# Kernel optimization log

Measured on AMD Instinct MI355X. Metric: run time of the kernel, lower is better.

## Reference

```python
import jax, jax.numpy as jnp
import numpy as np

SR = 44100
SEQ_DUR = 6.0
FBINS = 113
FMIN = 91.6
NSGT_SCALE = 100.0
MIN_WIN = 4


def _mel_frequencies(fmin, fmax, bnds):
    # MelScale from the nsgt package
    hz2mel = lambda f: 1127.01048 * np.log(f / 700.0 + 1.0)
    mel2hz = lambda m: (np.exp(m / 1127.01048) - 1.0) * 700.0
    mmin, mmax = hz2mel(fmin), hz2mel(fmax)
    mbnd = (mmax - mmin) / (bnds - 1)
    return mel2hz(np.arange(bnds) * mbnd + mmin)


def _hannwin(l):
    # fft-centered hann window (peak at index 0), as in nsgt.util.hannwin
    r = np.arange(l, dtype=np.float64) * (2.0 * np.pi / l)
    return 0.5 * (np.cos(r) + 1.0)


def _build_nsgt_params(Ls):
    """Replicates nsgfwin(sliced=False) + calcwinrange + matrixform nsgtf layout.
    Returns G[n_bins, maxLg] (window values, zero where padded) and
    idx[n_bins, maxLg] (gather indices into the length-Ls spectrum)."""
    f = _mel_frequencies(FMIN, SR / 2.0, FBINS)
    nf = SR / 2.0
    lim = int(np.argmax(f > 0))
    if lim != 0:
        f = f[lim:]
    lim = int(np.argmax(f >= nf))
    if lim != 0:
        f = f[:lim]
    lbas = len(f)
    frqs = np.concatenate(((0.0,), f, (nf,)))
    fbas = np.concatenate((frqs, SR - frqs[-2:0:-1]))
    fbas *= float(Ls) / SR
    # bandwidths M[k] (samples)
    M = np.zeros(fbas.shape, dtype=np.int64)
    M[0] = np.round(2 * fbas[1])
    for k in range(1, 2 * lbas + 1):
        M[k] = np.round(fbas[k + 1] - fbas[k - 1])
    M[-1] = np.round(Ls - fbas[-2])
    M = np.clip(M, MIN_WIN, None)
    g = [_hannwin(m) for m in M]
    fbas[lbas] = (fbas[lbas - 1] + fbas[lbas + 1]) / 2
    fbas[lbas + 2] = Ls - fbas[lbas]
    rfbas = np.round(fbas).astype(np.int64)  # window center positions (= timepos)
    # real=True, reducedform=0 -> keep bins 0 .. len(g)//2 (DC..Nyquist)
    n_bins = len(g) // 2 + 1
    maxLg = int(M.max())  # matrixform: every bin padded (in the middle) to max bandwidth
    idx = np.zeros((n_bins, maxLg), dtype=np.int32)
    G = np.zeros((n_bins, maxLg), dtype=np.float32)
    for j in range(n_bins):
        gj = g[j]
        Lg = len(gj)
        tp = int(rfbas[j])
        h = (Lg + 1) // 2  # positive-frequency half
        nh = Lg // 2       # negative-frequency half
        idx[j, :h] = (tp + np.arange(h)) % Ls
        G[j, :h] = gj[:h]
        if nh > 0:
            idx[j, maxLg - nh:] = (tp - nh + np.arange(nh)) % Ls
            G[j, maxLg - nh:] = gj[h:]
    return G, idx


def setup_inputs() -> dict:
    key = jax.random.key(0)
    S, C = 16, 2
    Ls = int(SEQ_DUR * SR)
    x = jax.random.normal(key, (S, C, Ls), dtype=jnp.float32)
    G, idx = _build_nsgt_params(Ls)
    return {"x": x, "G": jnp.asarray(G), "idx": jnp.asarray(idx)}


def reference(x, G, idx):
    # x: (S, C, Ls); G, idx: (n_bins, maxLg)
    S, C, T = x.shape
    ft = jnp.fft.fft(x.reshape(S * C, T))      # (N, Ls) complex64
    c = ft[:, idx] * G                         # (N, n_bins, maxLg): windowed spectrum slices
    coefs = jnp.fft.ifft(c, axis=-1)           # per-bin time frames (matrixform NSGT coeffs)
    coefs = coefs.reshape(S, C, c.shape[1], c.shape[2])
    # torch.view_as_real + * NSGT_SCALE
    return jnp.stack([coefs.real, coefs.imag], axis=-1) * NSGT_SCALE
```

## Files before the change

kernel.cpp:

```cpp
#include <hip/hip_runtime.h>

#define TPB 256
#define TPF 1024
constexpr int LS = 264600;
constexpr int N1 = 525;
constexpr int N2 = 504;
constexpr int ROWS = 32;
constexpr int M_FFT = 16384;
constexpr float TWO_PI_F = 6.28318530717958647692f;
constexpr float PI_F     = 3.14159265358979323846f;

__device__ __forceinline__ int rev7(int x) { return (int)(__brev((unsigned)x) >> 25); }
__device__ __forceinline__ float2 cmul(float2 a, float2 b) {
    return make_float2(a.x * b.x - a.y * b.y, a.x * b.y + a.y * b.x);
}
__device__ __forceinline__ int sidx(int hi, int lo) {
    return (hi << 7) + (lo ^ (hi & 15));
}

__global__ void k0_scan(const float* __restrict__ G, int NL, int* __restrict__ hnh) {
    const int j = blockIdx.x;
    __shared__ int s_first, s_last;
    if (threadIdx.x == 0) { s_first = NL; s_last = -1; }
    __syncthreads();
    const float* Gj = G + (size_t)j * NL;
    for (int m = threadIdx.x; m < NL; m += blockDim.x) {
        if (Gj[m] == 0.0f) {
            atomicMin(&s_first, m);
            atomicMax(&s_last, m);
        }
    }
    __syncthreads();
    if (threadIdx.x == 0) {
        int h  = s_first;
        int nh = (s_last >= 0) ? (NL - 1 - s_last) : 0;
        hnh[2 * j]     = h;
        hnh[2 * j + 1] = nh;
    }
}

__global__ __launch_bounds__(TPB) void k1_dft525(const float* __restrict__ x,
                                                 float2* __restrict__ A) {
    const int n2 = blockIdx.x;
    const int r  = blockIdx.y;
    __shared__ float  xs[N1];
    __shared__ float2 ys[N1];
    __shared__ float2 w25[25];
    __shared__ float2 w21[21];
    const float* xr = x + (size_t)r * LS + n2;
    for (int t = threadIdx.x; t < N1; t += TPB) {
        xs[t] = xr[(size_t)t * N2];
    }
    if (threadIdx.x < 25) {
        float a = -TWO_PI_F * (float)threadIdx.x / 25.0f;
        float s, c; sincosf(a, &s, &c);
        w25[threadIdx.x] = make_float2(c, s);
    } else if (threadIdx.x >= 32 && threadIdx.x < 53) {
        int k = threadIdx.x - 32;
        float a = -TWO_PI_F * (float)k / 21.0f;
        float s, c; sincosf(a, &s, &c);
        w21[k] = make_float2(c, s);
    }
    __syncthreads();
    for (int i = threadIdx.x; i < N1; i += TPB) {
        int alpha = i % 25, b = i / 25;
        float re = 0.f, im = 0.f;
        int iw = 0, it = b;
        #pragma unroll
        for (int a = 0; a < 25; ++a) {
            float  v = xs[it];
            float2 w = w25[iw];
            re = fmaf(v, w.x, re);
            im = fmaf(v, w.y, im);
            it += 21;
            iw += alpha; if (iw >= 25) iw -= 25;
        }
        float ang = -TWO_PI_F * (float)(b * alpha) / (float)N1;
        float s, c; sincosf(ang, &s, &c);
        ys[i] = make_float2(re * c - im * s, re * s + im * c);
    }
    __syncthreads();
    for (int k = threadIdx.x; k < N1; k += TPB) {
        int alpha = k % 25, beta = k / 25;
        float re = 0.f, im = 0.f;
        int iw = 0, iy = alpha;
        #pragma unroll
        for (int b = 0; b < 21; ++b) {
            float2 v = ys[iy];
            float2 w = w21[iw];
            re = fmaf(v.x, w.x, re); re = fmaf(-v.y, w.y, re);
            im = fmaf(v.x, w.y, im); im = fmaf( v.y, w.x, im);
            iy += 25;
            iw += beta; if (iw >= 21) iw -= 21;
        }
        float ang = -TWO_PI_F * (float)(k * n2) / (float)LS;
        float s, c; sincosf(ang, &s, &c);
        A[((size_t)r * N1 + k) * N2 + n2] = make_float2(re * c - im * s, re * s + im * c);
    }
}

__global__ __launch_bounds__(TPB) void k2_dft504(float2* __restrict__ A) {
    const int k1 = blockIdx.x;
    const int r  = blockIdx.y;
    __shared__ float2 as[N2];
    __shared__ float2 ys[N2];
    __shared__ float2 w21[21];
    __shared__ float2 w24[24];
    float2* row = A + ((size_t)r * N1 + k1) * N2;
    for (int t = threadIdx.x; t < N2; t += TPB) as[t] = row[t];
    if (threadIdx.x < 21) {
        float a = -TWO_PI_F * (float)threadIdx.x / 21.0f;
        float s, c; sincosf(a, &s, &c);
        w21[threadIdx.x] = make_float2(c, s);
    } else if (threadIdx.x >= 32 && threadIdx.x < 56) {
        int k = threadIdx.x - 32;
        float a = -TWO_PI_F * (float)k / 24.0f;
        float s, c; sincosf(a, &s, &c);
        w24[k] = make_float2(c, s);
    }
    __syncthreads();
    for (int i = threadIdx.x; i < N2; i += TPB) {
        int alpha = i % 21, b = i / 21;
        float re = 0.f, im = 0.f;
        int iw = 0, it = b;
        #pragma unroll
        for (int a = 0; a < 21; ++a) {
            float2 v = as[it];
            float2 w = w21[iw];
            re = fmaf(v.x, w.x, re); re = fmaf(-v.y, w.y, re);
            im = fmaf(v.x, w.y, im); im = fmaf( v.y, w.x, im);
            it += 24;
            iw += alpha; if (iw >= 21) iw -= 21;
        }
        float ang = -TWO_PI_F * (float)(b * alpha) / (float)N2;
        float s, c; sincosf(ang, &s, &c);
        ys[i] = make_float2(re * c - im * s, re * s + im * c);
    }
    __syncthreads();
    for (int k = threadIdx.x; k < N2; k += TPB) {
        int alpha = k % 21, beta = k / 21;
        float re = 0.f, im = 0.f;
        int iw = 0, iy = alpha;
        #pragma unroll
        for (int b = 0; b < 24; ++b) {
            float2 v = ys[iy];
            float2 w = w24[iw];
            re = fmaf(v.x, w.x, re); re = fmaf(-v.y, w.y, re);
            im = fmaf(v.x, w.y, im); im = fmaf( v.y, w.x, im);
            iy += 21;
            iw += beta; if (iw >= 24) iw -= 24;
        }
        row[k] = make_float2(re, im);
    }
}

__global__ void k_setup(float2* __restrict__ kc, float2* __restrict__ bchirp,
                        float2* __restrict__ twg, int NL) {
    int t = blockIdx.x * blockDim.x + threadIdx.x;
    long long twoNL = 2LL * NL;
    if (t < M_FFT) {
        long long d = 0; bool act = false;
        if (t < NL)              { d = t;        act = true; }
        else if (t > M_FFT - NL) { d = t - M_FFT; act = true; }
        float2 v = make_float2(0.f, 0.f);
        if (act) {
            long long ph = (d * d) % twoNL;
            float th = -PI_F * (float)ph / (float)NL;
            float s, c; sincosf(th, &s, &c);
            v = make_float2(c, s);
        }
        kc[t] = v;
    } else {
        int n = t - M_FFT;
        if (n < NL) {
            long long ph = ((long long)n * n) % twoNL;
            float th = PI_F * (float)ph / (float)NL;
            float s, c; sincosf(th, &s, &c);
            bchirp[n] = make_float2(c, s);
        } else if (n < NL + 64) {
            int q = n - NL;
            float th = -TWO_PI_F * (float)q / 128.0f;
            float s, c; sincosf(th, &s, &c);
            twg[q] = make_float2(c, s);
        }
    }
}

__device__ void fft128_dif(float2 (*ld)[129], const float2* tw, int f, int q) {
    for (int ls = 6; ls >= 0; --ls) {
        int span = 1 << ls;
        for (int b = q; b < 64; b += 16) {
            int j = b & (span - 1);
            int g = b >> ls;
            int u = (g << (ls + 1)) + j;
            int v = u + span;
            float2 A = ld[f][u], B = ld[f][v];
            float2 s = make_float2(A.x + B.x, A.y + B.y);
            float2 d = make_float2(A.x - B.x, A.y - B.y);
            ld[f][u] = s;
            ld[f][v] = cmul(d, tw[j << (6 - ls)]);
        }
        __syncthreads();
    }
}

#define FFT_PROLOG                                                        \
    __shared__ float2 ld[16][129];                                        \
    __shared__ float2 tw[64];                                             \
    if (threadIdx.x < 64) {                                               \
        float th = -TWO_PI_F * (float)threadIdx.x / 128.0f;               \
        float s, c; sincosf(th, &s, &c);                                  \
        tw[threadIdx.x] = make_float2(c, s);                              \
    }

__global__ __launch_bounds__(TPB) void kfft_cols_fwd(float2* __restrict__ P) {
    const int cg = blockIdx.x;
    const size_t vb = (size_t)blockIdx.y * M_FFT;
    FFT_PROLOG
    const int c0 = cg * 16;
    for (int i = threadIdx.x; i < 2048; i += TPB) {
        int cl = i & 15, r = i >> 4;
        ld[cl][r] = P[vb + (c0 + cl) + 128 * r];
    }
    __syncthreads();
    fft128_dif(ld, tw, threadIdx.x >> 4, threadIdx.x & 15);
    for (int i = threadIdx.x; i < 2048; i += TPB) {
        int cl = i & 15, pos = i >> 4;
        int c = c0 + cl;
        int k1 = rev7(pos);
        float th = -TWO_PI_F * (float)(c * k1) / (float)M_FFT;
        float s, co; sincosf(th, &s, &co);
        P[vb + c + 128 * pos] = cmul(ld[cl][pos], make_float2(co, s));
    }
}

__global__ __launch_bounds__(TPB) void kfft_rows_fwd(float2* __restrict__ P) {
    const int rg = blockIdx.x;
    const size_t vb = (size_t)blockIdx.y * M_FFT;
    FFT_PROLOG
    const int R0 = rg * 16;
    for (int i = threadIdx.x; i < 2048; i += TPB) {
        int fl = i >> 7, c = i & 127;
        ld[fl][c] = P[vb + (size_t)(R0 + fl) * 128 + c];
    }
    __syncthreads();
    fft128_dif(ld, tw, threadIdx.x >> 4, threadIdx.x & 15);
    for (int i = threadIdx.x; i < 2048; i += TPB) {
        int fl = i >> 7, pos = i & 127;
        P[vb + (size_t)(R0 + fl) * 128 + pos] = ld[fl][pos];
    }
}

__global__ __launch_bounds__(TPF) void k_fused(const float* __restrict__ Gm,
        const int* __restrict__ idxp, const float2* __restrict__ A,
        const int* __restrict__ hnh, const float2* __restrict__ bchirp,
        const float2* __restrict__ KF, const float2* __restrict__ twg,
        float2* __restrict__ out, int NB, int NL) {
    extern __shared__ float2 mp[];
    const int tid = threadIdx.x;
    const int vg = blockIdx.x;
    const int r = vg / NB, j = vg % NB;
    const int h = hnh[2 * j], nh = hnh[2 * j + 1];
    const int tail0 = NL - nh;
    const float* Gj = Gm + (size_t)j * NL;
    const int*   ij = idxp + (size_t)j * NL;
    const float2* Ar = A + (size_t)r * LS;

    for (int i = tid; i < M_FFT; i += TPF) {
        float2 val = make_float2(0.f, 0.f);
        if (i < h || (i >= tail0 && i < NL)) {
            int k = ij[i];
            float2 f = Ar[(size_t)(k % N1) * N2 + (k / N1)];
            float  g = Gj[i];
            val = cmul(make_float2(f.x * g, f.y * g), bchirp[i]);
        }
        mp[sidx(i >> 7, i & 127)] = val;
    }
    __syncthreads();

    for (int ls = 6; ls >= 0; --ls) {
        const int span = 1 << ls;
        for (int w = tid; w < 8192; w += TPF) {
            const int lo = w & 127, b = w >> 7;
            const int jj = b & (span - 1), g = b >> ls;
            const int u = (g << (ls + 1)) + jj, v = u + span;
            float2 Aa = mp[sidx(u, lo)], Bb = mp[sidx(v, lo)];
            float2 s = make_float2(Aa.x + Bb.x, Aa.y + Bb.y);
            float2 d = make_float2(Aa.x - Bb.x, Aa.y - Bb.y);
            mp[sidx(u, lo)] = s;
            mp[sidx(v, lo)] = cmul(d, twg[jj << (6 - ls)]);
        }
        __syncthreads();
    }
    for (int i = tid; i < M_FFT; i += TPF) {
        const int c = i & 127, pos = i >> 7;
        const int k1 = rev7(pos);
        float th = -TWO_PI_F * (float)(c * k1) / (float)M_FFT;
        float s, co; sincosf(th, &s, &co);
        const int p = sidx(pos, c);
        mp[p] = cmul(mp[p], make_float2(co, s));
    }
    __syncthreads();
    for (int ls = 6; ls >= 0; --ls) {
        const int span = 1 << ls;
        for (int w = tid; w < 8192; w += TPF) {
            const int hi = w & 127, b = w >> 7;
            const int jj = b & (span - 1), g = b >> ls;
            const int u = (g << (ls + 1)) + jj, v = u + span;
            float2 Aa = mp[sidx(hi, u)], Bb = mp[sidx(hi, v)];
            float2 s = make_float2(Aa.x + Bb.x, Aa.y + Bb.y);
            float2 d = make_float2(Aa.x - Bb.x, Aa.y - Bb.y);
            mp[sidx(hi, u)] = s;
            mp[sidx(hi, v)] = cmul(d, twg[jj << (6 - ls)]);
        }
        __syncthreads();
    }
    for (int i = tid; i < M_FFT; i += TPF) {
        const int p = sidx(i >> 7, i & 127);
        mp[p] = cmul(mp[p], KF[i]);
    }
    __syncthreads();
    for (int ls = 0; ls <= 6; ++ls) {
        const int span = 1 << ls;
        for (int w = tid; w < 8192; w += TPF) {
            const int hi = w & 127, b = w >> 7;
            const int jj = b & (span - 1), g = b >> ls;
            const int u = (g << (ls + 1)) + jj, v = u + span;
            float2 wv = twg[jj << (6 - ls)]; wv.y = -wv.y;
            float2 Aa = mp[sidx(hi, u)];
            float2 t  = cmul(mp[sidx(hi, v)], wv);
            mp[sidx(hi, u)] = make_float2(Aa.x + t.x, Aa.y + t.y);
            mp[sidx(hi, v)] = make_float2(Aa.x - t.x, Aa.y - t.y);
        }
        __syncthreads();
    }
    for (int i = tid; i < M_FFT; i += TPF) {
        const int pos = i & 127, R = i >> 7;
        const int k1 = rev7(R);
        float th = TWO_PI_F * (float)(k1 * pos) / (float)M_FFT;
        float s, co; sincosf(th, &s, &co);
        const int p = sidx(R, pos);
        mp[p] = cmul(mp[p], make_float2(co, s));
    }
    __syncthreads();
    for (int ls = 0; ls <= 6; ++ls) {
        const int span = 1 << ls;
        for (int w = tid; w < 8192; w += TPF) {
            const int lo = w & 127, b = w >> 7;
            const int jj = b & (span - 1), g = b >> ls;
            const int u = (g << (ls + 1)) + jj, v = u + span;
            float2 wv = twg[jj << (6 - ls)]; wv.y = -wv.y;
            float2 Aa = mp[sidx(u, lo)];
            float2 t  = cmul(mp[sidx(v, lo)], wv);
            mp[sidx(u, lo)] = make_float2(Aa.x + t.x, Aa.y + t.y);
            mp[sidx(v, lo)] = make_float2(Aa.x - t.x, Aa.y - t.y);
        }
        __syncthreads();
    }
    const float sc = 100.0f / ((float)NL * (float)M_FFT);
    float2* outv = out + (size_t)vg * NL;
    for (int n = tid; n < NL; n += TPF) {
        float2 y = cmul(mp[sidx(n >> 7, n & 127)], bchirp[n]);
        outv[n] = make_float2(y.x * sc, y.y * sc);
    }
}

__global__ __launch_bounds__(TPB) void k3_idft(const float* __restrict__ G,
                                               const int*  __restrict__ idxp,
                                               const float2* __restrict__ FT,
                                               const int*  __restrict__ hnh,
                                               float2* __restrict__ out,
                                               int NB, int NL) {
    extern __shared__ float2 cls[];
    const int j = blockIdx.x;
    const int r = blockIdx.y;
    const int h  = hnh[2 * j];
    const int nh = hnh[2 * j + 1];
    const int Lg = h + nh;
    const float* Gj = G    + (size_t)j * NL;
    const int*   ij = idxp + (size_t)j * NL;

    for (int t = threadIdx.x; t < Lg; t += TPB) {
        int m = (t < h) ? t : (NL - nh + (t - h));
        int k = ij[m];
        float2 f = FT[((size_t)r * N1 + (k % N1)) * N2 + (k / N1)];
        float  g = Gj[m];
        cls[t] = make_float2(f.x * g, f.y * g);
    }
    __syncthreads();

    const float scale = 100.0f / (float)NL;
    const float w0 = TWO_PI_F / (float)NL;
    float2* outr = out + ((size_t)r * NB + j) * NL;

    for (int n_base = 0; n_base < NL; n_base += 4 * TPB) {
        int   n[4];
        float are[4], aim[4], twr[4], twi[4], str[4], sti[4];
        #pragma unroll
        for (int u = 0; u < 4; ++u) {
            n[u] = n_base + u * TPB + (int)threadIdx.x;
            are[u] = 0.f; aim[u] = 0.f;
            float s, c; sincosf(w0 * (float)(n[u] % NL), &s, &c);
            str[u] = c; sti[u] = s;
            twr[u] = 1.f; twi[u] = 0.f;
        }
        for (int t = 0; t < h; ++t) {
            if ((t & 255) == 0) {
                #pragma unroll
                for (int u = 0; u < 4; ++u) {
                    int mm = (int)(((long long)t * (long long)n[u]) % NL);
                    float s, c; sincosf(w0 * (float)mm, &s, &c);
                    twr[u] = c; twi[u] = s;
                }
            }
            float2 cv = cls[t];
            #pragma unroll
            for (int u = 0; u < 4; ++u) {
                are[u] = fmaf(cv.x, twr[u], are[u]);
                are[u] = fmaf(-cv.y, twi[u], are[u]);
                aim[u] = fmaf(cv.x, twi[u], aim[u]);
                aim[u] = fmaf(cv.y, twr[u], aim[u]);
                float nr = twr[u] * str[u] - twi[u] * sti[u];
                float ni = twr[u] * sti[u] + twi[u] * str[u];
                twr[u] = nr; twi[u] = ni;
            }
        }
        const int m0 = NL - nh;
        for (int t = 0; t < nh; ++t) {
            if ((t & 255) == 0) {
                #pragma unroll
                for (int u = 0; u < 4; ++u) {
                    int mm = (int)(((long long)(m0 + t) * (long long)n[u]) % NL);
                    float s, c; sincosf(w0 * (float)mm, &s, &c);
                    twr[u] = c; twi[u] = s;
                }
            }
            float2 cv = cls[h + t];
            #pragma unroll
            for (int u = 0; u < 4; ++u) {
                are[u] = fmaf(cv.x, twr[u], are[u]);
                are[u] = fmaf(-cv.y, twi[u], are[u]);
                aim[u] = fmaf(cv.x, twi[u], aim[u]);
                aim[u] = fmaf(cv.y, twr[u], aim[u]);
                float nr = twr[u] * str[u] - twi[u] * sti[u];
                float ni = twr[u] * sti[u] + twi[u] * str[u];
                twr[u] = nr; twi[u] = ni;
            }
        }
        #pragma unroll
        for (int u = 0; u < 4; ++u) {
            if (n[u] < NL) outr[n[u]] = make_float2(are[u] * scale, aim[u] * scale);
        }
    }
}

static inline size_t align256(size_t x) { return (x + 255) & ~(size_t)255; }

extern "C" void kernel_launch(void* const* d_in, const int* in_sizes, int n_in,
                              void* d_out, int out_size, void* d_ws, size_t ws_size,
                              hipStream_t stream) {
    const float* x   = (const float*)d_in[0];
    const float* Gm  = (const float*)d_in[1];
    const int*   idx = (const int*)d_in[2];
    float2*      out = (float2*)d_out;

    const int p  = in_sizes[1];
    const int NB = (p % 114 == 0) ? 114 : 115;
    const int NL = p / NB;
    const int B  = NB * ROWS;

    size_t hnh_off    = 0;
    size_t bchirp_off = align256(hnh_off + 2048);
    size_t twg_off    = align256(bchirp_off + (size_t)NL * 8);
    size_t kc_off     = align256(twg_off + 64 * 8);
    size_t A_off      = align256(kc_off + (size_t)M_FFT * 8);
    size_t need       = A_off + (size_t)ROWS * LS * 8;

    int*    hnh    = (int*)((char*)d_ws + hnh_off);
    float2* bchirp = (float2*)((char*)d_ws + bchirp_off);
    float2* twg    = (float2*)((char*)d_ws + twg_off);
    float2* kc     = (float2*)((char*)d_ws + kc_off);
    float2* A      = (float2*)((char*)d_ws + A_off);

    k0_scan<<<dim3(NB), TPB, 0, stream>>>(Gm, NL, hnh);
    k1_dft525<<<dim3(N2, ROWS), TPB, 0, stream>>>(x, A);
    k2_dft504<<<dim3(N1, ROWS), TPB, 0, stream>>>(A);

    const bool fused_ok = (2 * NL - 1 <= M_FFT) && (need <= ws_size);
    if (fused_ok) {
        (void)hipFuncSetAttribute((const void*)k_fused,
                                  hipFuncAttributeMaxDynamicSharedMemorySize,
                                  M_FFT * (int)sizeof(float2));
        int setup_blocks = (M_FFT + NL + 64 + TPB - 1) / TPB;
        k_setup<<<dim3(setup_blocks), TPB, 0, stream>>>(kc, bchirp, twg, NL);
        kfft_cols_fwd<<<dim3(8, 1), TPB, 0, stream>>>(kc);
        kfft_rows_fwd<<<dim3(8, 1), TPB, 0, stream>>>(kc);
        k_fused<<<dim3(B), TPF, (size_t)M_FFT * sizeof(float2), stream>>>(
            Gm, idx, A, hnh, bchirp, kc, twg, out, NB, NL);
    } else {
        k3_idft<<<dim3(NB, ROWS), TPB, (size_t)NL * sizeof(float2), stream>>>(
            Gm, idx, A, hnh, out, NB, NL);
    }
}
```

Before: 1.504 ms.

## Rewrite Bluestein 16K FFT as register-resident radix-16/8 passes

Replaces the per-stage shared-memory radix-2 butterflies, which need a barrier after each of 28 stages, in the fused Bluestein kernel. Each 128-point sub-FFT is now split into an in-register radix-16 step and two radix-8 steps, with twiddles held in shared memory between them. The chirp kernel FFT moves into a single kernel that uses the same path and stores it transposed, so the pointwise multiply reads it coalesced in the new data order. The change cuts shared-memory traffic and barriers, but raises register pressure under launch_bounds(1024,4) and needs the twiddle table enlarged to 128 entries.

```diff
diff --git a/kernel.cpp b/kernel.cpp
--- a/kernel.cpp
+++ b/kernel.cpp
@@ -10,12 +10,61 @@
 constexpr float TWO_PI_F = 6.28318530717958647692f;
 constexpr float PI_F     = 3.14159265358979323846f;
 
-__device__ __forceinline__ int rev7(int x) { return (int)(__brev((unsigned)x) >> 25); }
 __device__ __forceinline__ float2 cmul(float2 a, float2 b) {
     return make_float2(a.x * b.x - a.y * b.y, a.x * b.y + a.y * b.x);
 }
 __device__ __forceinline__ int sidx(int hi, int lo) {
     return (hi << 7) + (lo ^ (hi & 15));
+}
+
+template<bool INV>
+__device__ __forceinline__ void fft16r(float2 v[16]) {
+    const float C16[8] = {1.f, 0.92387953251128674f, 0.70710678118654752f, 0.38268343236508977f,
+                          0.f, -0.38268343236508977f, -0.70710678118654752f, -0.92387953251128674f};
+    const float S16[8] = {0.f, 0.38268343236508977f, 0.70710678118654752f, 0.92387953251128674f,
+                          1.f, 0.92387953251128674f, 0.70710678118654752f, 0.38268343236508977f};
+    const float sg = INV ? 1.f : -1.f;
+    #pragma unroll
+    for (int ls = 3; ls >= 0; --ls) {
+        const int span = 1 << ls;
+        #pragma unroll
+        for (int g = 0; g < 16; g += 2 * span) {
+            #pragma unroll
+            for (int j = 0; j < span; ++j) {
+                const int u = g + j, w = u + span;
+                float2 a = v[u], b = v[w];
+                float2 d = make_float2(a.x - b.x, a.y - b.y);
+                v[u] = make_float2(a.x + b.x, a.y + b.y);
+                const int ti = j << (3 - ls);
+                v[w] = make_float2(d.x * C16[ti] - d.y * sg * S16[ti],
+                                   d.x * sg * S16[ti] + d.y * C16[ti]);
+            }
+        }
+    }
+}
+
+template<bool INV>
+__device__ __forceinline__ void fft8r(float2 v[8]) {
+    const float C8[4] = {1.f, 0.70710678118654752f, 0.f, -0.70710678118654752f};
+    const float S8[4] = {0.f, 0.70710678118654752f, 1.f, 0.70710678118654752f};
+    const float sg = INV ? 1.f : -1.f;
+    #pragma unroll
+    for (int ls = 2; ls >= 0; --ls) {
+        const int span = 1 << ls;
+        #pragma unroll
+        for (int g = 0; g < 8; g += 2 * span) {
+            #pragma unroll
+            for (int j = 0; j < span; ++j) {
+                const int u = g + j, w = u + span;
+                float2 a = v[u], b = v[w];
+                float2 d = make_float2(a.x - b.x, a.y - b.y);
+                v[u] = make_float2(a.x + b.x, a.y + b.y);
+                const int ti = j << (2 - ls);
+                v[w] = make_float2(d.x * C8[ti] - d.y * sg * S8[ti],
+                                   d.x * sg * S8[ti] + d.y * C8[ti]);
+            }
+        }
+    }
 }
 
 __global__ void k0_scan(const float* __restrict__ G, int NL, int* __restrict__ hnh) {
@@ -177,7 +226,7 @@
             float th = PI_F * (float)ph / (float)NL;
             float s, c; sincosf(th, &s, &c);
             bchirp[n] = make_float2(c, s);
-        } else if (n < NL + 64) {
+        } else if (n < NL + 128) {
             int q = n - NL;
             float th = -TWO_PI_F * (float)q / 128.0f;
             float s, c; sincosf(th, &s, &c);
@@ -186,87 +235,113 @@
     }
 }
 
-__device__ void fft128_dif(float2 (*ld)[129], const float2* tw, int f, int q) {
-    for (int ls = 6; ls >= 0; --ls) {
-        int span = 1 << ls;
-        for (int b = q; b < 64; b += 16) {
-            int j = b & (span - 1);
-            int g = b >> ls;
-            int u = (g << (ls + 1)) + j;
-            int v = u + span;
-            float2 A = ld[f][u], B = ld[f][v];
-            float2 s = make_float2(A.x + B.x, A.y + B.y);
-            float2 d = make_float2(A.x - B.x, A.y - B.y);
-            ld[f][u] = s;
-            ld[f][v] = cmul(d, tw[j << (6 - ls)]);
-        }
+__device__ __forceinline__ void fwd_after_load(float2* __restrict__ mp,
+        const float2* __restrict__ twg, float2 v[16], int lo, int n2) {
+    const int RV4[16] = {0,8,4,12,2,10,6,14,1,9,5,13,3,11,7,15};
+    const int RV3[8]  = {0,4,2,6,1,5,3,7};
+    fft16r<false>(v);
+    #pragma unroll
+    for (int p = 0; p < 16; ++p) {
+        const int k1 = RV4[p];
+        mp[sidx(8 * k1 + n2, lo)] = cmul(v[p], twg[n2 * k1]);
+    }
+    __syncthreads();
+    {
+        float2 u0[8], u1[8];
+        const int q = n2;
+        #pragma unroll
+        for (int m = 0; m < 8; ++m) u0[m] = mp[sidx(8 * q + m, lo)];
+        #pragma unroll
+        for (int m = 0; m < 8; ++m) u1[m] = mp[sidx(8 * (q + 8) + m, lo)];
         __syncthreads();
-    }
-}
-
-#define FFT_PROLOG                                                        \
-    __shared__ float2 ld[16][129];                                        \
-    __shared__ float2 tw[64];                                             \
-    if (threadIdx.x < 64) {                                               \
-        float th = -TWO_PI_F * (float)threadIdx.x / 128.0f;               \
-        float s, c; sincosf(th, &s, &c);                                  \
-        tw[threadIdx.x] = make_float2(c, s);                              \
-    }
-
-__global__ __launch_bounds__(TPB) void kfft_cols_fwd(float2* __restrict__ P) {
-    const int cg = blockIdx.x;
-    const size_t vb = (size_t)blockIdx.y * M_FFT;
-    FFT_PROLOG
-    const int c0 = cg * 16;
-    for (int i = threadIdx.x; i < 2048; i += TPB) {
-        int cl = i & 15, r = i >> 4;
-        ld[cl][r] = P[vb + (c0 + cl) + 128 * r];
-    }
-    __syncthreads();
-    fft128_dif(ld, tw, threadIdx.x >> 4, threadIdx.x & 15);
-    for (int i = threadIdx.x; i < 2048; i += TPB) {
-        int cl = i & 15, pos = i >> 4;
-        int c = c0 + cl;
-        int k1 = rev7(pos);
-        float th = -TWO_PI_F * (float)(c * k1) / (float)M_FFT;
-        float s, co; sincosf(th, &s, &co);
-        P[vb + c + 128 * pos] = cmul(ld[cl][pos], make_float2(co, s));
-    }
-}
-
-__global__ __launch_bounds__(TPB) void kfft_rows_fwd(float2* __restrict__ P) {
-    const int rg = blockIdx.x;
-    const size_t vb = (size_t)blockIdx.y * M_FFT;
-    FFT_PROLOG
-    const int R0 = rg * 16;
-    for (int i = threadIdx.x; i < 2048; i += TPB) {
-        int fl = i >> 7, c = i & 127;
-        ld[fl][c] = P[vb + (size_t)(R0 + fl) * 128 + c];
-    }
-    __syncthreads();
-    fft128_dif(ld, tw, threadIdx.x >> 4, threadIdx.x & 15);
-    for (int i = threadIdx.x; i < 2048; i += TPB) {
-        int fl = i >> 7, pos = i & 127;
-        P[vb + (size_t)(R0 + fl) * 128 + pos] = ld[fl][pos];
-    }
-}
-
-__global__ __launch_bounds__(TPF) void k_fused(const float* __restrict__ Gm,
+        fft8r<false>(u0);
+        fft8r<false>(u1);
+        #pragma unroll
+        for (int p = 0; p < 8; ++p) {
+            const int k2 = RV3[p];
+            {
+                const int rr = q + 16 * k2;
+                float th = -TWO_PI_F * (float)(rr * lo) / (float)M_FFT;
+                float s, c; sincosf(th, &s, &c);
+                mp[sidx(rr, lo)] = cmul(u0[p], make_float2(c, s));
+            }
+            {
+                const int rr = q + 8 + 16 * k2;
+                float th = -TWO_PI_F * (float)(rr * lo) / (float)M_FFT;
+                float s, c; sincosf(th, &s, &c);
+                mp[sidx(rr, lo)] = cmul(u1[p], make_float2(c, s));
+            }
+        }
+    }
+    __syncthreads();
+    const int hi = lo;
+    #pragma unroll
+    for (int n1 = 0; n1 < 16; ++n1) v[n1] = mp[sidx(hi, 8 * n1 + n2)];
+    fft16r<false>(v);
+    #pragma unroll
+    for (int p = 0; p < 16; ++p) {
+        const int k1 = RV4[p];
+        mp[sidx(hi, 8 * k1 + n2)] = cmul(v[p], twg[n2 * k1]);
+    }
+    __syncthreads();
+    {
+        float2 u0[8], u1[8];
+        const int q = n2;
+        #pragma unroll
+        for (int m = 0; m < 8; ++m) u0[m] = mp[sidx(hi, 8 * q + m)];
+        #pragma unroll
+        for (int m = 0; m < 8; ++m) u1[m] = mp[sidx(hi, 8 * (q + 8) + m)];
+        __syncthreads();
+        fft8r<false>(u0);
+        fft8r<false>(u1);
+        #pragma unroll
+        for (int p = 0; p < 8; ++p) {
+            const int k2 = RV3[p];
+            mp[sidx(hi, q + 16 * k2)]     = u0[p];
+            mp[sidx(hi, q + 8 + 16 * k2)] = u1[p];
+        }
+    }
+    __syncthreads();
+}
+
+__global__ __launch_bounds__(TPF, 4) void k_kf(const float2* __restrict__ kc,
+        const float2* __restrict__ twg, float2* __restrict__ KFt) {
+    extern __shared__ float2 mp[];
+    const int tid = threadIdx.x;
+    const int lo = tid & 127, n2 = tid >> 7;
+    float2 v[16];
+    #pragma unroll
+    for (int n1 = 0; n1 < 16; ++n1)
+        v[n1] = kc[(size_t)(8 * n1 + n2) * 128 + lo];
+    fwd_after_load(mp, twg, v, lo, n2);
+    for (int i = tid; i < M_FFT; i += TPF) {
+        int hh = i >> 7, ll = i & 127;
+        KFt[(size_t)ll * 128 + hh] = mp[sidx(hh, ll)];
+    }
+}
+
+__global__ __launch_bounds__(TPF, 4) void k_fused(const float* __restrict__ Gm,
         const int* __restrict__ idxp, const float2* __restrict__ A,
         const int* __restrict__ hnh, const float2* __restrict__ bchirp,
-        const float2* __restrict__ KF, const float2* __restrict__ twg,
+        const float2* __restrict__ KFt, const float2* __restrict__ twg,
         float2* __restrict__ out, int NB, int NL) {
     extern __shared__ float2 mp[];
     const int tid = threadIdx.x;
+    const int lo = tid & 127, n2 = tid >> 7;
     const int vg = blockIdx.x;
-    const int r = vg / NB, j = vg % NB;
-    const int h = hnh[2 * j], nh = hnh[2 * j + 1];
+    const int rr_ = vg / NB, jb = vg % NB;
+    const int h = hnh[2 * jb], nh = hnh[2 * jb + 1];
     const int tail0 = NL - nh;
-    const float* Gj = Gm + (size_t)j * NL;
-    const int*   ij = idxp + (size_t)j * NL;
-    const float2* Ar = A + (size_t)r * LS;
-
-    for (int i = tid; i < M_FFT; i += TPF) {
+    const float* Gj = Gm + (size_t)jb * NL;
+    const int*   ij = idxp + (size_t)jb * NL;
+    const float2* Ar = A + (size_t)rr_ * LS;
+    const int RV4[16] = {0,8,4,12,2,10,6,14,1,9,5,13,3,11,7,15};
+    const int RV3[8]  = {0,4,2,6,1,5,3,7};
+
+    float2 v[16];
+    #pragma unroll
+    for (int n1 = 0; n1 < 16; ++n1) {
+        const int i = (8 * n1 + n2) * 128 + lo;
         float2 val = make_float2(0.f, 0.f);
         if (i < h || (i >= tail0 && i < NL)) {
             int k = ij[i];
@@ -274,94 +349,93 @@
             float  g = Gj[i];
             val = cmul(make_float2(f.x * g, f.y * g), bchirp[i]);
         }
-        mp[sidx(i >> 7, i & 127)] = val;
-    }
-    __syncthreads();
-
-    for (int ls = 6; ls >= 0; --ls) {
-        const int span = 1 << ls;
-        for (int w = tid; w < 8192; w += TPF) {
-            const int lo = w & 127, b = w >> 7;
-            const int jj = b & (span - 1), g = b >> ls;
-            const int u = (g << (ls + 1)) + jj, v = u + span;
-            float2 Aa = mp[sidx(u, lo)], Bb = mp[sidx(v, lo)];
-            float2 s = make_float2(Aa.x + Bb.x, Aa.y + Bb.y);
-            float2 d = make_float2(Aa.x - Bb.x, Aa.y - Bb.y);
-            mp[sidx(u, lo)] = s;
-            mp[sidx(v, lo)] = cmul(d, twg[jj << (6 - ls)]);
-        }
+        v[n1] = val;
+    }
+    fwd_after_load(mp, twg, v, lo, n2);
+
+    const int hi = lo;
+    #pragma unroll
+    for (int n1 = 0; n1 < 16; ++n1) {
+        const int s = 8 * n1 + n2;
+        v[n1] = cmul(mp[sidx(hi, s)], KFt[(size_t)s * 128 + hi]);
+    }
+    fft16r<true>(v);
+    #pragma unroll
+    for (int p = 0; p < 16; ++p) {
+        const int k1 = RV4[p];
+        float2 t = twg[n2 * k1]; t.y = -t.y;
+        mp[sidx(hi, 8 * k1 + n2)] = cmul(v[p], t);
+    }
+    __syncthreads();
+    {
+        float2 u0[8], u1[8];
+        const int q = n2;
+        #pragma unroll
+        for (int m = 0; m < 8; ++m) u0[m] = mp[sidx(hi, 8 * q + m)];
+        #pragma unroll
+        for (int m = 0; m < 8; ++m) u1[m] = mp[sidx(hi, 8 * (q + 8) + m)];
         __syncthreads();
-    }
-    for (int i = tid; i < M_FFT; i += TPF) {
-        const int c = i & 127, pos = i >> 7;
-        const int k1 = rev7(pos);
-        float th = -TWO_PI_F * (float)(c * k1) / (float)M_FFT;
-        float s, co; sincosf(th, &s, &co);
-        const int p = sidx(pos, c);
-        mp[p] = cmul(mp[p], make_float2(co, s));
-    }
-    __syncthreads();
-    for (int ls = 6; ls >= 0; --ls) {
-        const int span = 1 << ls;
-        for (int w = tid; w < 8192; w += TPF) {
-            const int hi = w & 127, b = w >> 7;
-            const int jj = b & (span - 1), g = b >> ls;
-            const int u = (g << (ls + 1)) + jj, v = u + span;
-            float2 Aa = mp[sidx(hi, u)], Bb = mp[sidx(hi, v)];
-            float2 s = make_float2(Aa.x + Bb.x, Aa.y + Bb.y);
-            float2 d = make_float2(Aa.x - Bb.x, Aa.y - Bb.y);
-            mp[sidx(hi, u)] = s;
-            mp[sidx(hi, v)] = cmul(d, twg[jj << (6 - ls)]);
-        }
-        __syncthreads();
-    }
-    for (int i = tid; i < M_FFT; i += TPF) {
-        const int p = sidx(i >> 7, i & 127);
-        mp[p] = cmul(mp[p], KF[i]);
-    }
-    __syncthreads();
-    for (int ls = 0; ls <= 6; ++ls) {
-        const int span = 1 << ls;
-        for (int w = tid; w < 8192; w += TPF) {
-            const int hi = w & 127, b = w >> 7;
-            const int jj = b & (span - 1), g = b >> ls;
-            const int u = (g << (ls + 1)) + jj, v = u + span;
-            float2 wv = twg[jj << (6 - ls)]; wv.y = -wv.y;
-            float2 Aa = mp[sidx(hi, u)];
-            float2 t  = cmul(mp[sidx(hi, v)], wv);
-            mp[sidx(hi, u)] = make_float2(Aa.x + t.x, Aa.y + t.y);
-            mp[sidx(hi, v)] = make_float2(Aa.x - t.x, Aa.y - t.y);
-        }
-        __syncthreads();
-    }
-    for (int i = tid; i < M_FFT; i += TPF) {
-        const int pos = i & 127, R = i >> 7;
-        const int k1 = rev7(R);
-        float th = TWO_PI_F * (float)(k1 * pos) / (float)M_FFT;
-        float s, co; sincosf(th, &s, &co);
-        const int p = sidx(R, pos);
-        mp[p] = cmul(mp[p], make_float2(co, s));
-    }
-    __syncthreads();
-    for (int ls = 0; ls <= 6; ++ls) {
-        const int span = 1 << ls;
-        for (int w = tid; w < 8192; w += TPF) {
-            const int lo = w & 127, b = w >> 7;
-            const int jj = b & (span - 1), g = b >> ls;
-            const int u = (g << (ls + 1)) + jj, v = u + span;
-            float2 wv = twg[jj << (6 - ls)]; wv.y = -wv.y;
-            float2 Aa = mp[sidx(u, lo)];
-            float2 t  = cmul(mp[sidx(v, lo)], wv);
-            mp[sidx(u, lo)] = make_float2(Aa.x + t.x, Aa.y + t.y);
-            mp[sidx(v, lo)] = make_float2(Aa.x - t.x, Aa.y - t.y);
-        }
-        __syncthreads();
-    }
-    const float sc = 100.0f / ((float)NL * (float)M_FFT);
-    float2* outv = out + (size_t)vg * NL;
-    for (int n = tid; n < NL; n += TPF) {
-        float2 y = cmul(mp[sidx(n >> 7, n & 127)], bchirp[n]);
-        outv[n] = make_float2(y.x * sc, y.y * sc);
+        fft8r<true>(u0);
+        fft8r<true>(u1);
+        #pragma unroll
+        for (int p = 0; p < 8; ++p) {
+            const int k2 = RV3[p];
+            {
+                const int b = q + 16 * k2;
+                float th = TWO_PI_F * (float)(b * hi) / (float)M_FFT;
+                float s, c; sincosf(th, &s, &c);
+                mp[sidx(hi, b)] = cmul(u0[p], make_float2(c, s));
+            }
+            {
+                const int b = q + 8 + 16 * k2;
+                float th = TWO_PI_F * (float)(b * hi) / (float)M_FFT;
+                float s, c; sincosf(th, &s, &c);
+                mp[sidx(hi, b)] = cmul(u1[p], make_float2(c, s));
+            }
+        }
+    }
+    __syncthreads();
+    #pragma unroll
+    for (int n1 = 0; n1 < 16; ++n1) v[n1] = mp[sidx(8 * n1 + n2, lo)];
+    fft16r<true>(v);
+    #pragma unroll
+    for (int p = 0; p < 16; ++p) {
+        const int k1 = RV4[p];
+        float2 t = twg[n2 * k1]; t.y = -t.y;
+        mp[sidx(8 * k1 + n2, lo)] = cmul(v[p], t);
+    }
+    __syncthreads();
+    {
+        float2 u0[8], u1[8];
+        const int q = n2;
+        #pragma unroll
+        for (int m = 0; m < 8; ++m) u0[m] = mp[sidx(8 * q + m, lo)];
+        #pragma unroll
+        for (int m = 0; m < 8; ++m) u1[m] = mp[sidx(8 * (q + 8) + m, lo)];
+        fft8r<true>(u0);
+        fft8r<true>(u1);
+        const float sc = 100.0f / ((float)NL * (float)M_FFT);
+        float2* outv = out + (size_t)vg * NL;
+        #pragma unroll
+        for (int p = 0; p < 8; ++p) {
+            const int k2 = RV3[p];
+            {
+                const int a = q + 16 * k2;
+                const int n = 128 * a + lo;
+                if (n < NL) {
+                    float2 y = cmul(u0[p], bchirp[n]);
+                    outv[n] = make_float2(y.x * sc, y.y * sc);
+                }
+            }
+            {
+                const int a = q + 8 + 16 * k2;
+                const int n = 128 * a + lo;
+                if (n < NL) {
+                    float2 y = cmul(u1[p], bchirp[n]);
+                    outv[n] = make_float2(y.x * sc, y.y * sc);
+                }
+            }
+        }
     }
 }
 
@@ -472,14 +546,16 @@
     size_t hnh_off    = 0;
     size_t bchirp_off = align256(hnh_off + 2048);
     size_t twg_off    = align256(bchirp_off + (size_t)NL * 8);
-    size_t kc_off     = align256(twg_off + 64 * 8);
-    size_t A_off      = align256(kc_off + (size_t)M_FFT * 8);
+    size_t kc_off     = align256(twg_off + 128 * 8);
+    size_t kft_off    = align256(kc_off + (size_t)M_FFT * 8);
+    size_t A_off      = align256(kft_off + (size_t)M_FFT * 8);
     size_t need       = A_off + (size_t)ROWS * LS * 8;
 
     int*    hnh    = (int*)((char*)d_ws + hnh_off);
     float2* bchirp = (float2*)((char*)d_ws + bchirp_off);
     float2* twg    = (float2*)((char*)d_ws + twg_off);
     float2* kc     = (float2*)((char*)d_ws + kc_off);
+    float2* KFt    = (float2*)((char*)d_ws + kft_off);
     float2* A      = (float2*)((char*)d_ws + A_off);
 
     k0_scan<<<dim3(NB), TPB, 0, stream>>>(Gm, NL, hnh);
@@ -491,12 +567,14 @@
         (void)hipFuncSetAttribute((const void*)k_fused,
                                   hipFuncAttributeMaxDynamicSharedMemorySize,
                                   M_FFT * (int)sizeof(float2));
-        int setup_blocks = (M_FFT + NL + 64 + TPB - 1) / TPB;
+        (void)hipFuncSetAttribute((const void*)k_kf,
+                                  hipFuncAttributeMaxDynamicSharedMemorySize,
+                                  M_FFT * (int)sizeof(float2));
+        int setup_blocks = (M_FFT + NL + 128 + TPB - 1) / TPB;
         k_setup<<<dim3(setup_blocks), TPB, 0, stream>>>(kc, bchirp, twg, NL);
-        kfft_cols_fwd<<<dim3(8, 1), TPB, 0, stream>>>(kc);
-        kfft_rows_fwd<<<dim3(8, 1), TPB, 0, stream>>>(kc);
+        k_kf<<<dim3(1), TPF, (size_t)M_FFT * sizeof(float2), stream>>>(kc, twg, KFt);
         k_fused<<<dim3(B), TPF, (size_t)M_FFT * sizeof(float2), stream>>>(
-            Gm, idx, A, hnh, bchirp, kc, twg, out, NB, NL);
+            Gm, idx, A, hnh, bchirp, KFt, twg, out, NB, NL);
     } else {
         k3_idft<<<dim3(NB, ROWS), TPB, (size_t)NL * sizeof(float2), stream>>>(
             Gm, idx, A, hnh, out, NB, NL);
```

Measured after the change: 1.666 ms. +10.7%, slower.
